# Kernel optimization log

Hardware: AMD Instinct MI355X
Metric: run time of the kernel (lower is better)

Reference implementation:

```python
import jax, jax.numpy as jnp
import numpy as np

BN_EPS = 1e-5

def setup_inputs() -> dict:
    key = jax.random.key(0)
    k1, k2 = jax.random.split(key)
    B, C, H, W = 16, 256, 128, 128
    x = jax.random.normal(k1, (B, C, H, W), dtype=jnp.float32)
    w = jax.random.normal(k2, (C, 3), dtype=jnp.float32) * 0.1  # depthwise conv1d weight [c,1,3] squeezed
    gamma = jnp.ones((C,), dtype=jnp.float32)
    beta = jnp.zeros((C,), dtype=jnp.float32)
    running_mean = jnp.zeros((C,), dtype=jnp.float32)
    running_var = jnp.ones((C,), dtype=jnp.float32)
    return {"x": x, "w": w, "gamma": gamma, "beta": beta,
            "running_mean": running_mean, "running_var": running_var}


def reference(x, w, gamma, beta, running_mean, running_var):
    b, c, h, wd = x.shape
    xf = x.reshape(b, c, h * wd)
    mean = xf.mean(-1)                      # AdaptiveAvgPool2d(1)  -> [b,c]
    mx = xf.max(-1)                         # AdaptiveMaxPool2d(1)  -> [b,c]
    std = jnp.std(xf, axis=-1, ddof=1)      # torch std, unbiased   -> [b,c]
    u = jnp.stack([mean, mx, std], axis=-1)  # [b,c,3]
    # MS: per-batch median over the full [c,3] slice, then cube the deviation
    med = jnp.median(u.reshape(b, -1), axis=-1)  # [b]
    u = (u - med[:, None, None]) ** 3
    # depthwise Conv1d(k=3, groups=c) on length-3 input -> length-1 output
    z = jnp.einsum('bck,ck->bc', u, w)
    # BatchNorm1d (eval mode)
    z = (z - running_mean) * jax.lax.rsqrt(running_var + BN_EPS) * gamma + beta
    g = jax.nn.sigmoid(z)                    # [b,c]
    return x * g[:, :, None, None]
```

## Files before the change

### kernel.cpp

```cpp
#include <hip/hip_runtime.h>
#include <math.h>


typedef float fvec4 __attribute__((ext_vector_type(4)));

__global__ void stats_kernel(const float* __restrict__ x,
                             float* __restrict__ u, int HW) {
    const int bc  = blockIdx.x;
    const int tid = threadIdx.x;
    const float4* __restrict__ x4 =
        (const float4*)(x + (size_t)bc * (size_t)HW);
    const int n4 = HW >> 2;

    float s0 = 0.f, q0 = 0.f, m0 = -INFINITY;
    float s1 = 0.f, q1 = 0.f, m1 = -INFINITY;
    #pragma unroll 4
    for (int i = tid; i < n4; i += 512) {
        float4 v = x4[i];
        s0 += (v.x + v.y) + (v.z + v.w);
        q0 += (v.x * v.x + v.y * v.y) + (v.z * v.z + v.w * v.w);
        m0 = fmaxf(m0, fmaxf(fmaxf(v.x, v.y), fmaxf(v.z, v.w)));
        int j = i + 256;
        if (j < n4) {
            float4 w = x4[j];
            s1 += (w.x + w.y) + (w.z + w.w);
            q1 += (w.x * w.x + w.y * w.y) + (w.z * w.z + w.w * w.w);
            m1 = fmaxf(m1, fmaxf(fmaxf(w.x, w.y), fmaxf(w.z, w.w)));
        }
    }
    float s = s0 + s1, q = q0 + q1, mx = fmaxf(m0, m1);

    for (int off = 32; off > 0; off >>= 1) {
        s  += __shfl_down(s, off);
        q  += __shfl_down(q, off);
        mx  = fmaxf(mx, __shfl_down(mx, off));
    }
    __shared__ float ss[4], sq[4], sm[4];
    const int wid = tid >> 6, lane = tid & 63;
    if (lane == 0) { ss[wid] = s; sq[wid] = q; sm[wid] = mx; }
    __syncthreads();
    if (tid == 0) {
        float S = ss[0] + ss[1] + ss[2] + ss[3];
        float Q = sq[0] + sq[1] + sq[2] + sq[3];
        float M = fmaxf(fmaxf(sm[0], sm[1]), fmaxf(sm[2], sm[3]));
        float mean = S / (float)HW;
        float var  = (Q - S * mean) / (float)(HW - 1);
        var = fmaxf(var, 0.f);
        float* up = u + (size_t)bc * 3;
        up[0] = mean;
        up[1] = M;
        up[2] = sqrtf(var);
    }
}

__global__ void median_gate_kernel(const float* __restrict__ u,
                                   const float* __restrict__ w,
                                   const float* __restrict__ gamma,
                                   const float* __restrict__ beta,
                                   const float* __restrict__ rmean,
                                   const float* __restrict__ rvar,
                                   float* __restrict__ g, int C) {
    const int b   = blockIdx.x;
    const int tid = threadIdx.x;
    const int NV  = C * 3;
    __shared__ float sv[768];
    __shared__ float m0, m1;

    const float* ub = u + (size_t)b * NV;
    for (int i = tid; i < NV; i += 256) sv[i] = ub[i];
    __syncthreads();

    const int r0 = (NV - 1) / 2;
    const int r1 = NV / 2;
    for (int j = tid; j < NV; j += 256) {
        float v = sv[j];
        int lt = 0, eq = 0;
        for (int i = 0; i < NV; ++i) {
            float o = sv[i];
            lt += (o < v);
            eq += (o == v);
        }
        if (lt <= r0 && r0 < lt + eq) m0 = v;
        if (lt <= r1 && r1 < lt + eq) m1 = v;
    }
    __syncthreads();

    const float med = 0.5f * (m0 + m1);
    if (tid < C) {
        const int c = tid;
        float z = 0.f;
        #pragma unroll
        for (int k = 0; k < 3; ++k) {
            float d = sv[c * 3 + k] - med;
            z += (d * d * d) * w[c * 3 + k];
        }
        z = (z - rmean[c]) * rsqrtf(rvar[c] + 1e-5f) * gamma[c] + beta[c];
        g[(size_t)b * C + c] = 1.f / (1.f + expf(-z));
    }
}

__global__ void scale_kernel(const float* __restrict__ x,
                             const float* __restrict__ g,
                             float* __restrict__ out, int HW) {
    const int bc = blockIdx.x;
    const float gv = g[bc];
    const size_t base = (size_t)bc * (size_t)HW;
    const fvec4* __restrict__ x4 = (const fvec4*)(x + base);
    fvec4* __restrict__ o4 = (fvec4*)(out + base);
    const int n4 = HW >> 2;
    #pragma unroll 4
    for (int i = threadIdx.x; i < n4; i += 256) {
        fvec4 v = x4[i];
        v *= gv;
        __builtin_nontemporal_store(v, &o4[i]);
    }
}

extern "C" void kernel_launch(void* const* d_in, const int* in_sizes, int n_in,
                              void* d_out, int out_size, void* d_ws, size_t ws_size,
                              hipStream_t stream) {
    const float* x     = (const float*)d_in[0];
    const float* w     = (const float*)d_in[1];
    const float* gamma = (const float*)d_in[2];
    const float* beta  = (const float*)d_in[3];
    const float* rmean = (const float*)d_in[4];
    const float* rvar  = (const float*)d_in[5];
    float* out = (float*)d_out;

    const int C  = in_sizes[2];
    const int B  = 16;
    const int HW = in_sizes[0] / (B * C);

    float* u = (float*)d_ws;
    float* g = u + (size_t)B * C * 3;

    stats_kernel<<<B * C, 256, 0, stream>>>(x, u, HW);
    median_gate_kernel<<<B, 256, 0, stream>>>(u, w, gamma, beta, rmean, rvar, g, C);
    scale_kernel<<<B * C, 256, 0, stream>>>(x, g, out, HW);
}
```

Measured before the change: 158.1 us.

## Unroll stats loads, fuse median rank loops, reverse scale block order for cache reuse

The stats kernel gets a fully unrolled path for HW/4 == 4096 that issues 16 independent float4 loads per thread into four accumulator sets, raising memory-level parallelism. The median kernel counts ranks for three candidates in one pass over shared memory instead of three separate passes. The scale kernel walks channels in reverse order so it first reads the slices the stats kernel touched last, which may still be in the last-level cache. The median path now assumes exactly 768 values (C=256) and reads sv[tid+512] unguarded, so other channel counts would break.

Result: slower. 161.8 us (+2.3%).

```diff
diff --git a/kernel.cpp b/kernel.cpp
--- a/kernel.cpp
+++ b/kernel.cpp
@@ -14,21 +14,40 @@
 
     float s0 = 0.f, q0 = 0.f, m0 = -INFINITY;
     float s1 = 0.f, q1 = 0.f, m1 = -INFINITY;
-    #pragma unroll 4
-    for (int i = tid; i < n4; i += 512) {
-        float4 v = x4[i];
-        s0 += (v.x + v.y) + (v.z + v.w);
-        q0 += (v.x * v.x + v.y * v.y) + (v.z * v.z + v.w * v.w);
-        m0 = fmaxf(m0, fmaxf(fmaxf(v.x, v.y), fmaxf(v.z, v.w)));
-        int j = i + 256;
-        if (j < n4) {
-            float4 w = x4[j];
-            s1 += (w.x + w.y) + (w.z + w.w);
-            q1 += (w.x * w.x + w.y * w.y) + (w.z * w.z + w.w * w.w);
-            m1 = fmaxf(m1, fmaxf(fmaxf(w.x, w.y), fmaxf(w.z, w.w)));
+    float s2 = 0.f, q2 = 0.f, m2 = -INFINITY;
+    float s3 = 0.f, q3 = 0.f, m3 = -INFINITY;
+
+    if (n4 == 4096) {
+        #pragma unroll
+        for (int k = 0; k < 4; ++k) {
+            float4 a = x4[tid + (k * 4 + 0) * 256];
+            float4 b = x4[tid + (k * 4 + 1) * 256];
+            float4 c = x4[tid + (k * 4 + 2) * 256];
+            float4 d = x4[tid + (k * 4 + 3) * 256];
+            s0 += (a.x + a.y) + (a.z + a.w);
+            q0 += (a.x * a.x + a.y * a.y) + (a.z * a.z + a.w * a.w);
+            m0 = fmaxf(m0, fmaxf(fmaxf(a.x, a.y), fmaxf(a.z, a.w)));
+            s1 += (b.x + b.y) + (b.z + b.w);
+            q1 += (b.x * b.x + b.y * b.y) + (b.z * b.z + b.w * b.w);
+            m1 = fmaxf(m1, fmaxf(fmaxf(b.x, b.y), fmaxf(b.z, b.w)));
+            s2 += (c.x + c.y) + (c.z + c.w);
+            q2 += (c.x * c.x + c.y * c.y) + (c.z * c.z + c.w * c.w);
+            m2 = fmaxf(m2, fmaxf(fmaxf(c.x, c.y), fmaxf(c.z, c.w)));
+            s3 += (d.x + d.y) + (d.z + d.w);
+            q3 += (d.x * d.x + d.y * d.y) + (d.z * d.z + d.w * d.w);
+            m3 = fmaxf(m3, fmaxf(fmaxf(d.x, d.y), fmaxf(d.z, d.w)));
+        }
+    } else {
+        for (int i = tid; i < n4; i += 256) {
+            float4 a = x4[i];
+            s0 += (a.x + a.y) + (a.z + a.w);
+            q0 += (a.x * a.x + a.y * a.y) + (a.z * a.z + a.w * a.w);
+            m0 = fmaxf(m0, fmaxf(fmaxf(a.x, a.y), fmaxf(a.z, a.w)));
         }
     }
-    float s = s0 + s1, q = q0 + q1, mx = fmaxf(m0, m1);
+    float s = (s0 + s1) + (s2 + s3);
+    float q = (q0 + q1) + (q2 + q3);
+    float mx = fmaxf(fmaxf(m0, m1), fmaxf(m2, m3));
 
     for (int off = 32; off > 0; off >>= 1) {
         s  += __shfl_down(s, off);
@@ -64,28 +83,31 @@
     const int tid = threadIdx.x;
     const int NV  = C * 3;
     __shared__ float sv[768];
-    __shared__ float m0, m1;
+    __shared__ float ma, mb;
 
     const float* ub = u + (size_t)b * NV;
     for (int i = tid; i < NV; i += 256) sv[i] = ub[i];
     __syncthreads();
 
+    float v0 = sv[tid], v1 = sv[tid + 256], v2 = sv[tid + 512];
+    int lt0 = 0, eq0 = 0, lt1 = 0, eq1 = 0, lt2 = 0, eq2 = 0;
+    for (int i = 0; i < NV; ++i) {
+        float o = sv[i];
+        lt0 += (o < v0); eq0 += (o == v0);
+        lt1 += (o < v1); eq1 += (o == v1);
+        lt2 += (o < v2); eq2 += (o == v2);
+    }
     const int r0 = (NV - 1) / 2;
     const int r1 = NV / 2;
-    for (int j = tid; j < NV; j += 256) {
-        float v = sv[j];
-        int lt = 0, eq = 0;
-        for (int i = 0; i < NV; ++i) {
-            float o = sv[i];
-            lt += (o < v);
-            eq += (o == v);
-        }
-        if (lt <= r0 && r0 < lt + eq) m0 = v;
-        if (lt <= r1 && r1 < lt + eq) m1 = v;
-    }
+    if (lt0 <= r0 && r0 < lt0 + eq0) ma = v0;
+    if (lt1 <= r0 && r0 < lt1 + eq1) ma = v1;
+    if (lt2 <= r0 && r0 < lt2 + eq2) ma = v2;
+    if (lt0 <= r1 && r1 < lt0 + eq0) mb = v0;
+    if (lt1 <= r1 && r1 < lt1 + eq1) mb = v1;
+    if (lt2 <= r1 && r1 < lt2 + eq2) mb = v2;
     __syncthreads();
 
-    const float med = 0.5f * (m0 + m1);
+    const float med = 0.5f * (ma + mb);
     if (tid < C) {
         const int c = tid;
         float z = 0.f;
@@ -102,7 +124,7 @@
 __global__ void scale_kernel(const float* __restrict__ x,
                              const float* __restrict__ g,
                              float* __restrict__ out, int HW) {
-    const int bc = blockIdx.x;
+    const int bc = (int)gridDim.x - 1 - (int)blockIdx.x;
     const float gv = g[bc];
     const size_t base = (size_t)bc * (size_t)HW;
     const fvec4* __restrict__ x4 = (const fvec4*)(x + base);
```
